# Optimization experiments

Hardware: AMD Instinct MI355X
Metric: run time of the kernel (lower is better)

Reference implementation:

```python
import jax, jax.numpy as jnp
import numpy as np

B, TQ, TKV, D, H = 4, 512, 4096, 1024, 8
HEAD_DIM = D // H


def setup_inputs() -> dict:
    key = jax.random.key(0)
    ks = jax.random.split(key, 8)
    s = 0.02
    inputs_q = jax.random.normal(ks[0], (B, TQ, D), jnp.float32)
    inputs_kv = jax.random.normal(ks[1], (B, TKV, D), jnp.float32)
    attention_mask = jax.random.randint(ks[2], (B, TQ, TKV), 0, 2).astype(bool)
    Wq = jax.random.normal(ks[3], (D, D), jnp.float32) * s
    Wk = jax.random.normal(ks[4], (D, D), jnp.float32) * s
    Wv = jax.random.normal(ks[5], (D, D), jnp.float32) * s
    Wo = jax.random.normal(ks[6], (D, D), jnp.float32) * s
    zb = jnp.zeros((D,), jnp.float32)
    return {"inputs_q": inputs_q, "inputs_kv": inputs_kv, "attention_mask": attention_mask,
            "Wq": Wq, "bq": zb, "Wk": Wk, "bk": zb, "Wv": Wv, "bv": zb, "Wo": Wo, "bo": zb}


def _split_heads(x, h):
    b, t, c = x.shape
    return x.reshape(b, t, h, c // h).transpose(0, 2, 1, 3)  # b h t d


def reference(inputs_q, inputs_kv, attention_mask, Wq, bq, Wk, bk, Wv, bv, Wo, bo):
    q = _split_heads(inputs_q @ Wq + bq, H)   # [b,h,tq,d]
    k = _split_heads(inputs_kv @ Wk + bk, H)  # [b,h,tkv,d]
    v = _split_heads(inputs_kv @ Wv + bv, H)  # [b,h,tkv,d]
    scale = 1.0 / np.sqrt(HEAD_DIM).astype(np.float32)
    scores = jnp.einsum('bhtd,bhTd->bhtT', q, k) * scale
    large_k = jnp.asarray(1e30, scores.dtype)  # 1e30 for fp32 per source
    scores = jnp.where(attention_mask[:, None, :, :], scores, -large_k)
    probs = jax.nn.softmax(scores, axis=-1)
    summed = jnp.einsum('bhtT,bhTd->bhtd', probs, v)
    b, h, t, d = summed.shape
    summed = summed.transpose(0, 2, 1, 3).reshape(b, t, h * d)  # [b,tq,hiddens]
    # wipe rows whose mask is entirely zero (post-softmax wipe-masking)
    wipe = jnp.all(~attention_mask, axis=-1, keepdims=True)  # [b,tq,1]
    summed = jnp.where(wipe, jnp.zeros_like(summed), summed)
    return summed @ Wo + bo
```

## Files before the change

kernel.cpp:

```cpp
#include <hip/hip_runtime.h>
#include <cstdint>
#include <cstddef>

typedef unsigned short US;
typedef __bf16 bf16_t;
typedef bf16_t bf16x8 __attribute__((ext_vector_type(8)));
typedef float  f32x4  __attribute__((ext_vector_type(4)));
typedef US     us8    __attribute__((ext_vector_type(8)));
typedef US     us4    __attribute__((ext_vector_type(4)));

#define AS1 __attribute__((address_space(1)))
#define AS3 __attribute__((address_space(3)))

__device__ __forceinline__ void gl_lds16(const void* g, void* l) {
    __builtin_amdgcn_global_load_lds((AS1 unsigned int*)(size_t)g,
                                     (AS3 unsigned int*)l, 16, 0, 0);
}

__device__ __forceinline__ US f2bf(float f) {
    unsigned u = __builtin_bit_cast(unsigned, f);
    u += 0x7FFFu + ((u >> 16) & 1u);
    return (US)(u >> 16);
}

__device__ __forceinline__ bf16x8 ldv8(const US* p) {
    return __builtin_bit_cast(bf16x8, *(const us8*)p);
}

__global__ void prep(const float* __restrict__ Xq, const float* __restrict__ Xkv,
                     const int* __restrict__ Mi, US* __restrict__ XqB,
                     US* __restrict__ XkvB, US* __restrict__ MB) {
    int b = blockIdx.x, tid = threadIdx.x;
    if (b < 2048) {
        int i = b * 256 + tid;
        float4 f = ((const float4*)Xq)[i];
        us4 o = { f2bf(f.x), f2bf(f.y), f2bf(f.z), f2bf(f.w) };
        ((us4*)XqB)[i] = o;
    } else if (b < 18432) {
        int i = (b - 2048) * 256 + tid;
        float4 f = ((const float4*)Xkv)[i];
        us4 o = { f2bf(f.x), f2bf(f.y), f2bf(f.z), f2bf(f.w) };
        ((us4*)XkvB)[i] = o;
    } else {
        int i = (b - 18432) * 256 + tid;
        int4 m = ((const int4*)Mi)[i];
        us4 o = { (US)(m.x ? 1 : 0), (US)(m.y ? 1 : 0),
                  (US)(m.z ? 1 : 0), (US)(m.w ? 1 : 0) };
        ((us4*)MB)[i] = o;
    }
}

__global__ void wt_conv(const float* __restrict__ Wq, const float* __restrict__ Wk,
                        const float* __restrict__ Wv, const float* __restrict__ Wo,
                        US* __restrict__ outbase) {
    const float* W = (blockIdx.z == 0) ? Wq : (blockIdx.z == 1) ? Wk
                   : (blockIdx.z == 2) ? Wv : Wo;
    US* WT = outbase + (size_t)blockIdx.z * 1024 * 1024;
    __shared__ float t[32][33];
    int tx = threadIdx.x & 31, ty = threadIdx.x >> 5;
    int x = blockIdx.x * 32 + tx;
#pragma unroll
    for (int r = 0; r < 4; ++r)
        t[ty + r * 8][tx] = W[(size_t)(blockIdx.y * 32 + ty + r * 8) * 1024 + x];
    __syncthreads();
    int nx = blockIdx.y * 32 + tx;
#pragma unroll
    for (int r = 0; r < 4; ++r)
        WT[(size_t)(blockIdx.x * 32 + ty + r * 8) * 1024 + nx] = f2bf(t[tx][ty + r * 8]);
}

__global__ void v_transpose(const US* __restrict__ Vh, US* __restrict__ VTh) {
    __shared__ US t[32][33];
    int tx = threadIdx.x & 31, ty = threadIdx.x >> 5;
    size_t base = (size_t)blockIdx.z * 4096 * 128;
    int t0 = blockIdx.x * 32, d0 = blockIdx.y * 32;
#pragma unroll
    for (int r = 0; r < 4; ++r)
        t[ty + r * 8][tx] = Vh[base + (size_t)(t0 + ty + r * 8) * 128 + d0 + tx];
    __syncthreads();
#pragma unroll
    for (int r = 0; r < 4; ++r)
        VTh[base + (size_t)(d0 + ty + r * 8) * 4096 + t0 + tx] = t[tx][ty + r * 8];
}

template <int MODE>
__global__ __launch_bounds__(256, 2)
void gemm_bt(const US* __restrict__ A, const US* __restrict__ Bt,
             const float* __restrict__ bias, void* __restrict__ out,
             int tlog2, float scale) {
    constexpr int K = 1024, N = 1024, BK = 64;
    __shared__ US As[128 * BK];
    __shared__ US Bs[128 * BK];
    const int tid = threadIdx.x;
    const int wv = tid >> 6, ln = tid & 63;
    const int g = ln >> 4, c15 = ln & 15;
    const int m0 = blockIdx.x * 128, n0 = blockIdx.y * 128;
    const int wm = (wv & 1) * 64, wn = (wv >> 1) * 64;

    f32x4 acc[4][4];
    const f32x4 z = {0.f, 0.f, 0.f, 0.f};
#pragma unroll
    for (int i = 0; i < 4; ++i)
#pragma unroll
        for (int j = 0; j < 4; ++j) acc[i][j] = z;

    const US* Ab = A + (size_t)m0 * K;
    const US* Bb = Bt + (size_t)n0 * K;

    for (int k0 = 0; k0 < K; k0 += BK) {
        __syncthreads();
#pragma unroll
        for (int q = 0; q < 4; ++q) {
            int eb = (q * 256 + wv * 64) * 8;
            int r = (eb >> 6) + (ln >> 3);
            int sw = (ln & 7) ^ (r & 7);
            gl_lds16(Ab + (size_t)r * K + k0 + sw * 8, &As[eb]);
            gl_lds16(Bb + (size_t)r * K + k0 + sw * 8, &Bs[eb]);
        }
        __syncthreads();
#pragma unroll
        for (int ks = 0; ks < 2; ++ks) {
            bf16x8 a[4], b[4];
#pragma unroll
            for (int i = 0; i < 4; ++i) {
                int p = (ks * 4 + g) ^ (c15 & 7);
                a[i] = ldv8(&As[(wm + i * 16 + c15) * BK + p * 8]);
            }
#pragma unroll
            for (int j = 0; j < 4; ++j) {
                int p = (ks * 4 + g) ^ (c15 & 7);
                b[j] = ldv8(&Bs[(wn + j * 16 + c15) * BK + p * 8]);
            }
#pragma unroll
            for (int i = 0; i < 4; ++i)
#pragma unroll
                for (int j = 0; j < 4; ++j)
                    acc[i][j] = __builtin_amdgcn_mfma_f32_16x16x32_bf16(a[i], b[j], acc[i][j], 0, 0, 0);
        }
    }

#pragma unroll
    for (int i = 0; i < 4; ++i) {
#pragma unroll
        for (int j = 0; j < 4; ++j) {
            int col = n0 + wn + j * 16 + c15;
            float bvv = bias[col];
#pragma unroll
            for (int r = 0; r < 4; ++r) {
                int row = m0 + wm + i * 16 + g * 4 + r;
                float v = (acc[i][j][r] + bvv) * scale;
                if (MODE == 0) {
                    int b_ = row >> tlog2;
                    int t = row & ((1 << tlog2) - 1);
                    int h = col >> 7, d = col & 127;
                    ((US*)out)[(((size_t)(b_ * 8 + h) << tlog2) + t) * 128 + d] = f2bf(v);
                } else {
                    ((float*)out)[(size_t)row * N + col] = v;
                }
            }
        }
    }
}

__global__ __launch_bounds__(256, 2)
void gemm_kv(const US* __restrict__ A, const US* __restrict__ BtK,
             const US* __restrict__ BtV, const float* __restrict__ bk,
             const float* __restrict__ bv, US* __restrict__ Kout,
             US* __restrict__ Vout) {
    constexpr int K = 1024, BK = 64;
    __shared__ US As[128 * BK];
    __shared__ US BsK[128 * BK];
    __shared__ US BsV[128 * BK];
    const int tid = threadIdx.x;
    const int wv = tid >> 6, ln = tid & 63;
    const int g = ln >> 4, c15 = ln & 15;
    const int m0 = blockIdx.x * 128, n0 = blockIdx.y * 128;
    const int wm = (wv & 1) * 64, wn = (wv >> 1) * 64;

    f32x4 aK[4][4], aV[4][4];
    const f32x4 z = {0.f, 0.f, 0.f, 0.f};
#pragma unroll
    for (int i = 0; i < 4; ++i)
#pragma unroll
        for (int j = 0; j < 4; ++j) { aK[i][j] = z; aV[i][j] = z; }

    const US* Ab  = A   + (size_t)m0 * K;
    const US* BbK = BtK + (size_t)n0 * K;
    const US* BbV = BtV + (size_t)n0 * K;

    for (int k0 = 0; k0 < K; k0 += BK) {
        __syncthreads();
#pragma unroll
        for (int q = 0; q < 4; ++q) {
            int eb = (q * 256 + wv * 64) * 8;
            int r = (eb >> 6) + (ln >> 3);
            int sw = (ln & 7) ^ (r & 7);
            gl_lds16(Ab  + (size_t)r * K + k0 + sw * 8, &As[eb]);
            gl_lds16(BbK + (size_t)r * K + k0 + sw * 8, &BsK[eb]);
            gl_lds16(BbV + (size_t)r * K + k0 + sw * 8, &BsV[eb]);
        }
        __syncthreads();
#pragma unroll
        for (int ks = 0; ks < 2; ++ks) {
            bf16x8 a[4], bK[4], bV[4];
#pragma unroll
            for (int i = 0; i < 4; ++i) {
                int p = (ks * 4 + g) ^ (c15 & 7);
                a[i] = ldv8(&As[(wm + i * 16 + c15) * BK + p * 8]);
            }
#pragma unroll
            for (int j = 0; j < 4; ++j) {
                int p = (ks * 4 + g) ^ (c15 & 7);
                bK[j] = ldv8(&BsK[(wn + j * 16 + c15) * BK + p * 8]);
                bV[j] = ldv8(&BsV[(wn + j * 16 + c15) * BK + p * 8]);
            }
#pragma unroll
            for (int i = 0; i < 4; ++i)
#pragma unroll
                for (int j = 0; j < 4; ++j) {
                    aK[i][j] = __builtin_amdgcn_mfma_f32_16x16x32_bf16(a[i], bK[j], aK[i][j], 0, 0, 0);
                    aV[i][j] = __builtin_amdgcn_mfma_f32_16x16x32_bf16(a[i], bV[j], aV[i][j], 0, 0, 0);
                }
        }
    }

#pragma unroll
    for (int i = 0; i < 4; ++i) {
#pragma unroll
        for (int j = 0; j < 4; ++j) {
            int col = n0 + wn + j * 16 + c15;
            float bkv = bk[col], bvv = bv[col];
            int h = col >> 7, d = col & 127;
#pragma unroll
            for (int r = 0; r < 4; ++r) {
                int row = m0 + wm + i * 16 + g * 4 + r;
                int b_ = row >> 12, t = row & 4095;
                size_t oi = (((size_t)(b_ * 8 + h) << 12) + t) * 128 + d;
                Kout[oi] = f2bf(aK[i][j][r] + bkv);
                Vout[oi] = f2bf(aV[i][j][r] + bvv);
            }
        }
    }
}

__global__ __launch_bounds__(256, 3)
void flash(const US* __restrict__ Qh, const US* __restrict__ Kh,
           const US* __restrict__ VTh, const US* __restrict__ Mk,
           float* __restrict__ Opart, float* __restrict__ Lpart) {
    __shared__ US Ks[64 * 128];
    __shared__ US Vs[128 * 64];
    __shared__ US Ps[4][32 * 64];
    const int tid = threadIdx.x, wv = tid >> 6, ln = tid & 63;
    const int g = ln >> 4, c15 = ln & 15;
    const int qt = blockIdx.x, qbase = qt * 128;
    const int bh = blockIdx.y, b_ = bh >> 3;
    const int sp = blockIdx.z;
    const int t0 = (sp < 4) ? sp * 11 : 44 + (sp - 4) * 10;
    const int nt = (sp < 4) ? 11 : 10;
    const int wq = wv * 32;

    bf16x8 qa[2][4];
#pragma unroll
    for (int ib = 0; ib < 2; ++ib) {
        const US* qrow = Qh + ((size_t)bh * 512 + qbase + wq + ib * 16 + c15) * 128;
#pragma unroll
        for (int ks = 0; ks < 4; ++ks)
            qa[ib][ks] = ldv8(qrow + ks * 32 + g * 8);
    }

    f32x4 o[8][2];
    const f32x4 z = {0.f, 0.f, 0.f, 0.f};
#pragma unroll
    for (int d = 0; d < 8; ++d) { o[d][0] = z; o[d][1] = z; }
    float l2[2] = {0.f, 0.f};

    const US* mp[2];
    mp[0] = Mk + (size_t)(b_ * 512 + qbase + wq + c15) * 4096;
    mp[1] = mp[0] + (size_t)16 * 4096;
    const US* Kbase = Kh + ((size_t)bh * 4096 + (size_t)t0 * 64) * 128;
    const US* Vbase = VTh + (size_t)bh * 128 * 4096;
    US* Pw = &Ps[wv][0];

    for (int t = 0; t < nt; ++t) {
        int kv0 = (t0 + t) * 64;
        __syncthreads();
        const US* Kb = Kbase + (size_t)t * 64 * 128;
#pragma unroll
        for (int q = 0; q < 4; ++q) {
            int eb = (q * 256 + wv * 64) * 8;
            int r = (eb >> 7) + (ln >> 4);
            int sw = (ln & 15) ^ (r & 15);
            gl_lds16(Kb + (size_t)r * 128 + sw * 8, &Ks[eb]);
        }
#pragma unroll
        for (int q = 0; q < 4; ++q) {
            int eb = (q * 256 + wv * 64) * 8;
            int r = (eb >> 6) + (ln >> 3);
            int sw = (ln & 7) ^ (r & 7);
            gl_lds16(Vbase + (size_t)r * 4096 + kv0 + sw * 8, &Vs[eb]);
        }
        us4 mv[2][4];
#pragma unroll
        for (int ib = 0; ib < 2; ++ib)
#pragma unroll
            for (int kb = 0; kb < 4; ++kb)
                mv[ib][kb] = *(const us4*)(mp[ib] + kv0 + kb * 16 + g * 4);
        __syncthreads();

#pragma unroll
        for (int kb = 0; kb < 4; ++kb) {
            f32x4 s0 = z, s1 = z;
#pragma unroll
            for (int ks = 0; ks < 4; ++ks) {
                bf16x8 kf = ldv8(&Ks[(kb * 16 + c15) * 128 + (((ks * 4 + g) ^ c15) * 8)]);
                s0 = __builtin_amdgcn_mfma_f32_16x16x32_bf16(kf, qa[0][ks], s0, 0, 0, 0);
                s1 = __builtin_amdgcn_mfma_f32_16x16x32_bf16(kf, qa[1][ks], s1, 0, 0, 0);
            }
            int cw = kb * 4 + g;
#pragma unroll
            for (int ib = 0; ib < 2; ++ib) {
                f32x4 sv = ib ? s1 : s0;
                float p0 = mv[ib][kb].x ? __expf(sv[0]) : 0.f;
                float p1 = mv[ib][kb].y ? __expf(sv[1]) : 0.f;
                float p2 = mv[ib][kb].z ? __expf(sv[2]) : 0.f;
                float p3 = mv[ib][kb].w ? __expf(sv[3]) : 0.f;
                l2[ib] += (p0 + p1) + (p2 + p3);
                int q = ib * 16 + c15;
                US* wp = Pw + q * 64 + (((cw >> 1) ^ (q & 7)) * 8) + (cw & 1) * 4;
                us4 pv = { f2bf(p0), f2bf(p1), f2bf(p2), f2bf(p3) };
                *(us4*)wp = pv;
            }
        }

#pragma unroll
        for (int ks = 0; ks < 2; ++ks) {
            bf16x8 pf[2];
#pragma unroll
            for (int ib = 0; ib < 2; ++ib) {
                int q = ib * 16 + c15;
                pf[ib] = ldv8(&Pw[q * 64 + (((ks * 4 + g) ^ (q & 7)) * 8)]);
            }
#pragma unroll
            for (int d = 0; d < 8; ++d) {
                bf16x8 vf = ldv8(&Vs[(d * 16 + c15) * 64 + (((ks * 4 + g) ^ (c15 & 7)) * 8)]);
                o[d][0] = __builtin_amdgcn_mfma_f32_16x16x32_bf16(vf, pf[0], o[d][0], 0, 0, 0);
                o[d][1] = __builtin_amdgcn_mfma_f32_16x16x32_bf16(vf, pf[1], o[d][1], 0, 0, 0);
            }
        }
    }

    float lf[2];
#pragma unroll
    for (int ib = 0; ib < 2; ++ib) {
        float l = l2[ib];
        l += __shfl_xor(l, 16); l += __shfl_xor(l, 32);
        lf[ib] = l;
    }
    if (ln < 16) {
        size_t lb = ((size_t)sp * 32 + bh) * 512 + qbase + wq + c15;
        Lpart[lb] = lf[0];
        Lpart[lb + 16] = lf[1];
    }
    float* Ob = Opart + (((size_t)sp * 32 + bh) * 128 + g * 4) * 512 + qbase + wq + c15;
#pragma unroll
    for (int d = 0; d < 8; ++d)
#pragma unroll
        for (int r = 0; r < 4; ++r) {
            Ob[(size_t)(d * 16 + r) * 512] = o[d][0][r];
            Ob[(size_t)(d * 16 + r) * 512 + 16] = o[d][1][r];
        }
}

__global__ void combine(const float* __restrict__ Opart, const float* __restrict__ Lpart,
                        US* __restrict__ AO) {
    __shared__ float linv[128];
    __shared__ float T[128 * 33];
    const int qt = blockIdx.x, bh = blockIdx.y;
    const int b_ = bh >> 3, h = bh & 7;
    const int tid = threadIdx.x;
    const size_t spstride = (size_t)32 * 128 * 512;

    if (tid < 128) {
        float s = 0.f;
#pragma unroll
        for (int sp = 0; sp < 6; ++sp)
            s += Lpart[((size_t)sp * 32 + bh) * 512 + qt * 128 + tid];
        linv[tid] = (s > 0.f) ? 1.f / s : 0.f;
    }
    __syncthreads();

    for (int ds0 = 0; ds0 < 128; ds0 += 32) {
        if (ds0) __syncthreads();
#pragma unroll
        for (int it = 0; it < 4; ++it) {
            int d = ds0 + (tid >> 5) + it * 8, qc = tid & 31;
            const float* base = Opart + ((size_t)bh * 128 + d) * 512 + qt * 128 + qc * 4;
            float4 a = {0.f, 0.f, 0.f, 0.f};
#pragma unroll
            for (int sp = 0; sp < 6; ++sp) {
                float4 v = *(const float4*)(base + sp * spstride);
                a.x += v.x; a.y += v.y; a.z += v.z; a.w += v.w;
            }
            int dd = d - ds0;
            T[(qc * 4 + 0) * 33 + dd] = a.x * linv[qc * 4 + 0];
            T[(qc * 4 + 1) * 33 + dd] = a.y * linv[qc * 4 + 1];
            T[(qc * 4 + 2) * 33 + dd] = a.z * linv[qc * 4 + 2];
            T[(qc * 4 + 3) * 33 + dd] = a.w * linv[qc * 4 + 3];
        }
        __syncthreads();
#pragma unroll
        for (int it = 0; it < 4; ++it) {
            int idx = tid + it * 256;
            int q = idx >> 3, c = idx & 7;
            const float* tr = &T[q * 33 + c * 4];
            us4 ov = { f2bf(tr[0]), f2bf(tr[1]), f2bf(tr[2]), f2bf(tr[3]) };
            *(us4*)(AO + ((size_t)(b_ * 512 + qt * 128 + q)) * 1024 + h * 128 + ds0 + c * 4) = ov;
        }
    }
}

extern "C" void kernel_launch(void* const* d_in, const int* in_sizes, int n_in,
                              void* d_out, int out_size, void* d_ws, size_t ws_size,
                              hipStream_t stream) {
    (void)in_sizes; (void)n_in; (void)out_size; (void)ws_size;
    const float* Xq  = (const float*)d_in[0];
    const float* Xkv = (const float*)d_in[1];
    const int*   Mi  = (const int*)d_in[2];
    const float* Wq  = (const float*)d_in[3];
    const float* bq  = (const float*)d_in[4];
    const float* Wk  = (const float*)d_in[5];
    const float* bk  = (const float*)d_in[6];
    const float* Wv  = (const float*)d_in[7];
    const float* bv  = (const float*)d_in[8];
    const float* Wo  = (const float*)d_in[9];
    const float* bo  = (const float*)d_in[10];
    float* out = (float*)d_out;

    char* p = (char*)d_ws;
    US* WT   = (US*)p; p += (size_t)4 * 1024 * 1024 * 2;
    US* AO   = (US*)p; p += (size_t)2048 * 1024 * 2;
    US* XqB  = (US*)p; p += (size_t)2048 * 1024 * 2;
    US* Qh   = (US*)p; p += (size_t)2048 * 1024 * 2;
    US* Kh   = (US*)p; p += (size_t)16384 * 1024 * 2;
    US* VTh  = (US*)p; p += (size_t)16384 * 1024 * 2;
    US* XkvB = (US*)p; p += (size_t)16384 * 1024 * 2;
    US* Vh   = (US*)p; p += (size_t)16384 * 1024 * 2;
    US* MB   = (US*)p; p += (size_t)4 * 512 * 4096 * 2;
    float* Opart = (float*)XkvB;
    float* Lpart = (float*)XqB;

    prep<<<26624, 256, 0, stream>>>(Xq, Xkv, Mi, XqB, XkvB, MB);
    wt_conv<<<dim3(32, 32, 4), 256, 0, stream>>>(Wq, Wk, Wv, Wo, WT);

    gemm_bt<0><<<dim3(16, 8), 256, 0, stream>>>(XqB, WT, bq, Qh, 9, 0.08838834764831843f);
    gemm_kv<<<dim3(128, 8), 256, 0, stream>>>(XkvB, WT + 1048576, WT + 2097152,
                                              bk, bv, Kh, Vh);
    v_transpose<<<dim3(128, 4, 32), 256, 0, stream>>>(Vh, VTh);
    flash<<<dim3(4, 32, 6), 256, 0, stream>>>(Qh, Kh, VTh, MB, Opart, Lpart);
    combine<<<dim3(4, 32), 256, 0, stream>>>(Opart, Lpart, AO);
    gemm_bt<1><<<dim3(16, 8), 256, 0, stream>>>(AO, WT + 3145728, bo, out, 0, 1.0f);
}
```

Before: 353.6 us.

## Bit-pack attention mask, fuse V transpose into KV GEMM, shrink Q/O GEMM tiles

```diff
diff --git a/kernel.cpp b/kernel.cpp
--- a/kernel.cpp
+++ b/kernel.cpp
@@ -29,7 +29,7 @@
 
 __global__ void prep(const float* __restrict__ Xq, const float* __restrict__ Xkv,
                      const int* __restrict__ Mi, US* __restrict__ XqB,
-                     US* __restrict__ XkvB, US* __restrict__ MB) {
+                     US* __restrict__ XkvB, unsigned long long* __restrict__ MBits) {
     int b = blockIdx.x, tid = threadIdx.x;
     if (b < 2048) {
         int i = b * 256 + tid;
@@ -43,10 +43,9 @@
         ((us4*)XkvB)[i] = o;
     } else {
         int i = (b - 18432) * 256 + tid;
-        int4 m = ((const int4*)Mi)[i];
-        us4 o = { (US)(m.x ? 1 : 0), (US)(m.y ? 1 : 0),
-                  (US)(m.z ? 1 : 0), (US)(m.w ? 1 : 0) };
-        ((us4*)MB)[i] = o;
+        int m = Mi[i];
+        unsigned long long bits = __ballot(m != 0);
+        if ((tid & 63) == 0) MBits[i >> 6] = bits;
     }
 }
 
@@ -69,38 +68,25 @@
         WT[(size_t)(blockIdx.x * 32 + ty + r * 8) * 1024 + nx] = f2bf(t[tx][ty + r * 8]);
 }
 
-__global__ void v_transpose(const US* __restrict__ Vh, US* __restrict__ VTh) {
-    __shared__ US t[32][33];
-    int tx = threadIdx.x & 31, ty = threadIdx.x >> 5;
-    size_t base = (size_t)blockIdx.z * 4096 * 128;
-    int t0 = blockIdx.x * 32, d0 = blockIdx.y * 32;
-#pragma unroll
-    for (int r = 0; r < 4; ++r)
-        t[ty + r * 8][tx] = Vh[base + (size_t)(t0 + ty + r * 8) * 128 + d0 + tx];
-    __syncthreads();
-#pragma unroll
-    for (int r = 0; r < 4; ++r)
-        VTh[base + (size_t)(d0 + ty + r * 8) * 4096 + t0 + tx] = t[tx][ty + r * 8];
-}
-
-template <int MODE>
+template <int MODE, int BM>
 __global__ __launch_bounds__(256, 2)
 void gemm_bt(const US* __restrict__ A, const US* __restrict__ Bt,
              const float* __restrict__ bias, void* __restrict__ out,
              int tlog2, float scale) {
     constexpr int K = 1024, N = 1024, BK = 64;
-    __shared__ US As[128 * BK];
+    constexpr int MI = BM / 32;
+    __shared__ US As[BM * BK];
     __shared__ US Bs[128 * BK];
     const int tid = threadIdx.x;
     const int wv = tid >> 6, ln = tid & 63;
     const int g = ln >> 4, c15 = ln & 15;
-    const int m0 = blockIdx.x * 128, n0 = blockIdx.y * 128;
-    const int wm = (wv & 1) * 64, wn = (wv >> 1) * 64;
-
-    f32x4 acc[4][4];
+    const int m0 = blockIdx.x * BM, n0 = blockIdx.y * 128;
+    const int wm = (wv & 1) * (BM / 2), wn = (wv >> 1) * 64;
+
+    f32x4 acc[MI][4];
     const f32x4 z = {0.f, 0.f, 0.f, 0.f};
 #pragma unroll
-    for (int i = 0; i < 4; ++i)
+    for (int i = 0; i < MI; ++i)
 #pragma unroll
         for (int j = 0; j < 4; ++j) acc[i][j] = z;
 
@@ -109,20 +95,26 @@
 
     for (int k0 = 0; k0 < K; k0 += BK) {
         __syncthreads();
+#pragma unroll
+        for (int q = 0; q < BM / 32; ++q) {
+            int eb = (q * 256 + wv * 64) * 8;
+            int r = (eb >> 6) + (ln >> 3);
+            int sw = (ln & 7) ^ (r & 7);
+            gl_lds16(Ab + (size_t)r * K + k0 + sw * 8, &As[eb]);
+        }
 #pragma unroll
         for (int q = 0; q < 4; ++q) {
             int eb = (q * 256 + wv * 64) * 8;
             int r = (eb >> 6) + (ln >> 3);
             int sw = (ln & 7) ^ (r & 7);
-            gl_lds16(Ab + (size_t)r * K + k0 + sw * 8, &As[eb]);
             gl_lds16(Bb + (size_t)r * K + k0 + sw * 8, &Bs[eb]);
         }
         __syncthreads();
 #pragma unroll
         for (int ks = 0; ks < 2; ++ks) {
-            bf16x8 a[4], b[4];
-#pragma unroll
-            for (int i = 0; i < 4; ++i) {
+            bf16x8 a[MI], b[4];
+#pragma unroll
+            for (int i = 0; i < MI; ++i) {
                 int p = (ks * 4 + g) ^ (c15 & 7);
                 a[i] = ldv8(&As[(wm + i * 16 + c15) * BK + p * 8]);
             }
@@ -132,7 +124,7 @@
                 b[j] = ldv8(&Bs[(wn + j * 16 + c15) * BK + p * 8]);
             }
 #pragma unroll
-            for (int i = 0; i < 4; ++i)
+            for (int i = 0; i < MI; ++i)
 #pragma unroll
                 for (int j = 0; j < 4; ++j)
                     acc[i][j] = __builtin_amdgcn_mfma_f32_16x16x32_bf16(a[i], b[j], acc[i][j], 0, 0, 0);
@@ -140,7 +132,7 @@
     }
 
 #pragma unroll
-    for (int i = 0; i < 4; ++i) {
+    for (int i = 0; i < MI; ++i) {
 #pragma unroll
         for (int j = 0; j < 4; ++j) {
             int col = n0 + wn + j * 16 + c15;
@@ -166,11 +158,12 @@
 void gemm_kv(const US* __restrict__ A, const US* __restrict__ BtK,
              const US* __restrict__ BtV, const float* __restrict__ bk,
              const float* __restrict__ bv, US* __restrict__ Kout,
-             US* __restrict__ Vout) {
+             US* __restrict__ VTout) {
     constexpr int K = 1024, BK = 64;
-    __shared__ US As[128 * BK];
-    __shared__ US BsK[128 * BK];
-    __shared__ US BsV[128 * BK];
+    __shared__ US lds[3 * 128 * BK];
+    US* As  = lds;
+    US* BsK = lds + 128 * BK;
+    US* BsV = lds + 2 * 128 * BK;
     const int tid = threadIdx.x;
     const int wv = tid >> 6, ln = tid & 63;
     const int g = ln >> 4, c15 = ln & 15;
@@ -224,28 +217,54 @@
         }
     }
 
+    const int h = n0 >> 7;
+    const int b_ = m0 >> 12, tbase = m0 & 4095;
+
 #pragma unroll
     for (int i = 0; i < 4; ++i) {
 #pragma unroll
         for (int j = 0; j < 4; ++j) {
             int col = n0 + wn + j * 16 + c15;
-            float bkv = bk[col], bvv = bv[col];
-            int h = col >> 7, d = col & 127;
+            float bkv = bk[col];
+            int d = col & 127;
 #pragma unroll
             for (int r = 0; r < 4; ++r) {
                 int row = m0 + wm + i * 16 + g * 4 + r;
-                int b_ = row >> 12, t = row & 4095;
-                size_t oi = (((size_t)(b_ * 8 + h) << 12) + t) * 128 + d;
-                Kout[oi] = f2bf(aK[i][j][r] + bkv);
-                Vout[oi] = f2bf(aV[i][j][r] + bvv);
-            }
-        }
+                int t = row & 4095;
+                Kout[(((size_t)(b_ * 8 + h) << 12) + t) * 128 + d] = f2bf(aK[i][j][r] + bkv);
+            }
+        }
+    }
+
+    __syncthreads();
+    US* T = lds;
+#pragma unroll
+    for (int i = 0; i < 4; ++i) {
+#pragma unroll
+        for (int j = 0; j < 4; ++j) {
+            int dcol = wn + j * 16 + c15;
+            float bvv = bv[n0 + dcol];
+#pragma unroll
+            for (int r = 0; r < 4; ++r) {
+                int kvrow = wm + i * 16 + g * 4 + r;
+                T[dcol * 136 + kvrow] = f2bf(aV[i][j][r] + bvv);
+            }
+        }
+    }
+    __syncthreads();
+    {
+        int d = tid >> 1, half = (tid & 1) * 64;
+        US* vrow = VTout + ((size_t)(b_ * 8 + h) * 128 + d) * 4096 + tbase + half;
+        const US* tr = &T[d * 136 + half];
+#pragma unroll
+        for (int s = 0; s < 8; ++s)
+            *(us8*)(vrow + s * 8) = *(const us8*)(tr + s * 8);
     }
 }
 
 __global__ __launch_bounds__(256, 3)
 void flash(const US* __restrict__ Qh, const US* __restrict__ Kh,
-           const US* __restrict__ VTh, const US* __restrict__ Mk,
+           const US* __restrict__ VTh, const unsigned long long* __restrict__ MBits,
            float* __restrict__ Opart, float* __restrict__ Lpart) {
     __shared__ US Ks[64 * 128];
     __shared__ US Vs[128 * 64];
@@ -274,9 +293,9 @@
     for (int d = 0; d < 8; ++d) { o[d][0] = z; o[d][1] = z; }
     float l2[2] = {0.f, 0.f};
 
-    const US* mp[2];
-    mp[0] = Mk + (size_t)(b_ * 512 + qbase + wq + c15) * 4096;
-    mp[1] = mp[0] + (size_t)16 * 4096;
+    const unsigned long long* Mrow[2];
+    Mrow[0] = MBits + (size_t)(b_ * 512 + qbase + wq + c15) * 64;
+    Mrow[1] = Mrow[0] + (size_t)16 * 64;
     const US* Kbase = Kh + ((size_t)bh * 4096 + (size_t)t0 * 64) * 128;
     const US* Vbase = VTh + (size_t)bh * 128 * 4096;
     US* Pw = &Ps[wv][0];
@@ -299,12 +318,9 @@
             int sw = (ln & 7) ^ (r & 7);
             gl_lds16(Vbase + (size_t)r * 4096 + kv0 + sw * 8, &Vs[eb]);
         }
-        us4 mv[2][4];
-#pragma unroll
-        for (int ib = 0; ib < 2; ++ib)
-#pragma unroll
-            for (int kb = 0; kb < 4; ++kb)
-                mv[ib][kb] = *(const us4*)(mp[ib] + kv0 + kb * 16 + g * 4);
+        unsigned long long m64[2];
+        m64[0] = Mrow[0][t0 + t];
+        m64[1] = Mrow[1][t0 + t];
         __syncthreads();
 
 #pragma unroll
@@ -320,10 +336,11 @@
 #pragma unroll
             for (int ib = 0; ib < 2; ++ib) {
                 f32x4 sv = ib ? s1 : s0;
-                float p0 = mv[ib][kb].x ? __expf(sv[0]) : 0.f;
-                float p1 = mv[ib][kb].y ? __expf(sv[1]) : 0.f;
-                float p2 = mv[ib][kb].z ? __expf(sv[2]) : 0.f;
-                float p3 = mv[ib][kb].w ? __expf(sv[3]) : 0.f;
+                unsigned mq = (unsigned)(m64[ib] >> (kb * 16 + g * 4)) & 15u;
+                float p0 = (mq & 1u) ? __expf(sv[0]) : 0.f;
+                float p1 = (mq & 2u) ? __expf(sv[1]) : 0.f;
+                float p2 = (mq & 4u) ? __expf(sv[2]) : 0.f;
+                float p3 = (mq & 8u) ? __expf(sv[3]) : 0.f;
                 l2[ib] += (p0 + p1) + (p2 + p3);
                 int q = ib * 16 + c15;
                 US* wp = Pw + q * 64 + (((cw >> 1) ^ (q & 7)) * 8) + (cw & 1) * 4;
@@ -444,19 +461,19 @@
     US* Kh   = (US*)p; p += (size_t)16384 * 1024 * 2;
     US* VTh  = (US*)p; p += (size_t)16384 * 1024 * 2;
     US* XkvB = (US*)p; p += (size_t)16384 * 1024 * 2;
-    US* Vh   = (US*)p; p += (size_t)16384 * 1024 * 2;
-    US* MB   = (US*)p; p += (size_t)4 * 512 * 4096 * 2;
+    char* OT = p;      p += (size_t)4 * 1024 * 1024 * 4;
+    unsigned long long* MBits = (unsigned long long*)p; p += (size_t)131072 * 8;
+    (void)OT;
     float* Opart = (float*)XkvB;
     float* Lpart = (float*)XqB;
 
-    prep<<<26624, 256, 0, stream>>>(Xq, Xkv, Mi, XqB, XkvB, MB);
+    prep<<<51200, 256, 0, stream>>>(Xq, Xkv, Mi, XqB, XkvB, MBits);
     wt_conv<<<dim3(32, 32, 4), 256, 0, stream>>>(Wq, Wk, Wv, Wo, WT);
 
-    gemm_bt<0><<<dim3(16, 8), 256, 0, stream>>>(XqB, WT, bq, Qh, 9, 0.08838834764831843f);
+    gemm_bt<0, 64><<<dim3(32, 8), 256, 0, stream>>>(XqB, WT, bq, Qh, 9, 0.08838834764831843f);
     gemm_kv<<<dim3(128, 8), 256, 0, stream>>>(XkvB, WT + 1048576, WT + 2097152,
-                                              bk, bv, Kh, Vh);
-    v_transpose<<<dim3(128, 4, 32), 256, 0, stream>>>(Vh, VTh);
-    flash<<<dim3(4, 32, 6), 256, 0, stream>>>(Qh, Kh, VTh, MB, Opart, Lpart);
+                                              bk, bv, Kh, VTh);
+    flash<<<dim3(4, 32, 6), 256, 0, stream>>>(Qh, Kh, VTh, MBits, Opart, Lpart);
     combine<<<dim3(4, 32), 256, 0, stream>>>(Opart, Lpart, AO);
-    gemm_bt<1><<<dim3(16, 8), 256, 0, stream>>>(AO, WT + 3145728, bo, out, 0, 1.0f);
-}
+    gemm_bt<1, 64><<<dim3(32, 8), 256, 0, stream>>>(AO, WT + 3145728, bo, out, 0, 1.0f);
+}
```

After: 351.9 us. About the same (-0.5%).
